# Performance work log

Hardware: AMD Instinct MI355X
Metric: run time of the kernel (lower is better)

## Reference

```python
import jax, jax.numpy as jnp
import numpy as np

NU = 30000   # n_users
NI = 15000   # n_items
D = 64       # embed_dim (== layer widths)
R = 5        # ratingClass == ratingSocial
NU5 = NU * R
NI5 = NI * R
NADJ = NU + NI5
NNZ_S = 1_200_000
NNZ_A = 840_000


def _spmm(rows, cols, vals, x, n_rows):
    # sparse (COO) matrix @ dense: out[r] = sum_e vals[e] * x[cols[e]] for rows[e]==r
    return jax.ops.segment_sum(vals[:, None] * x[cols], rows, num_segments=n_rows)


def _prelu(x, alpha):
    return jnp.where(x >= 0, x, alpha[0] * x)


def setup_inputs() -> dict:
    key = jax.random.key(0)
    ks = jax.random.split(key, 12)
    sc = lambda fan: 1.0 / np.sqrt(fan)
    return {
        "user_emb": 0.1 * jax.random.normal(ks[0], (NU5, D), jnp.float32),
        "item_emb": 0.1 * jax.random.normal(ks[1], (NI5, D), jnp.float32),
        "w_r1_w": sc(2 * D) * jax.random.normal(ks[2], (D, 2 * D), jnp.float32),
        "w_r1_b": jnp.zeros((D,), jnp.float32),
        "social_w1": sc(D) * jax.random.normal(ks[3], (D, D), jnp.float32),
        "user_w1": sc(D) * jax.random.normal(ks[4], (D, D), jnp.float32),
        "item_w1": sc(D) * jax.random.normal(ks[5], (D, D), jnp.float32),
        "alpha": jnp.full((1,), 0.25, jnp.float32),  # PReLU default init
        "social_vals": jax.random.uniform(ks[6], (NNZ_S,), jnp.float32) / 8.0,
        "adj_vals": jax.random.uniform(ks[7], (NNZ_A,), jnp.float32) / 8.0,
        "social_rows": jax.random.randint(ks[8], (NNZ_S,), 0, NU5, jnp.int32),
        "social_cols": jax.random.randint(ks[9], (NNZ_S,), 0, NU5, jnp.int32),
        "adj_rows": jax.random.randint(ks[10], (NNZ_A,), 0, NADJ, jnp.int32),
        "adj_cols": jax.random.randint(ks[11], (NNZ_A,), 0, NADJ, jnp.int32),
    }


def reference(user_emb, item_emb, w_r1_w, w_r1_b, social_w1, user_w1, item_w1,
              alpha, social_vals, adj_vals, social_rows, social_cols,
              adj_rows, adj_cols):
    # --- getSocialEmbedding ---
    e0 = _prelu(_spmm(social_rows, social_cols, social_vals, user_emb, NU5), alpha)
    e1 = _prelu(_spmm(social_rows, social_cols, social_vals, e0 @ social_w1, NU5), alpha)
    u_multi = jnp.concatenate([e0, e1], axis=1)            # (NU5, 128)
    u_social = u_multi.reshape(NU, R, 2 * D).sum(axis=1) / 4.0  # (NU, 128)

    # --- forward ---
    u = u_social @ w_r1_w.T + w_r1_b                        # Linear(128 -> 64)
    ego = jnp.concatenate([u, item_emb], axis=0)            # (NADJ, 64)
    emb = _prelu(_spmm(adj_rows, adj_cols, adj_vals, ego, NADJ), alpha)
    au0, ai0 = emb[:NU], emb[NU:]
    ego1 = jnp.concatenate([au0 @ user_w1, ai0 @ item_w1], axis=0)
    emb1 = _prelu(_spmm(adj_rows, adj_cols, adj_vals, ego1, NADJ), alpha)
    au1, ai1 = emb1[:NU], emb1[NU:]

    user_embedding = jnp.concatenate([au0, au1], axis=1)    # (NU, 128)
    item_multi = jnp.concatenate([ai0, ai1], axis=1)        # (NI5, 128)
    item_embedding = item_multi.reshape(NI, R, 2 * D).sum(axis=1) / 5.0
    return (user_embedding, item_embedding)
```

## Files before the change

### kernel.cpp

```cpp
#include <hip/hip_runtime.h>
#include <hip/hip_bf16.h>

#define NUu 30000
#define NIi 15000
#define DD 64
#define RR 5
#define NU5 150000
#define NI5 75000
#define NADJ 105000
#define NNZ_S 1200000
#define NNZ_A 840000

#define SCAN_TPB 256
#define SCAN_ELEMS 8
#define SCAN_CHUNK (SCAN_TPB * SCAN_ELEMS)

#define NBK 256
#define CHUNK 2048
#define CAP_S 10240
#define CAP_A 5120
#define NBUCK_S ((NU5 + 1023) >> 10)
#define NBUCK_A ((NADJ + 511) >> 9)

__global__ void scan_partial(const int* __restrict__ counts, int n,
                             int* __restrict__ ptr, int* __restrict__ blocksums) {
    __shared__ int sh[SCAN_TPB];
    int base = blockIdx.x * SCAN_CHUNK;
    int t = threadIdx.x;
    int loc[SCAN_ELEMS];
    int s = 0;
#pragma unroll
    for (int i = 0; i < SCAN_ELEMS; ++i) {
        int idx = base + t * SCAN_ELEMS + i;
        int v = (idx < n) ? counts[idx] : 0;
        loc[i] = s;
        s += v;
    }
    sh[t] = s;
    __syncthreads();
    for (int off = 1; off < SCAN_TPB; off <<= 1) {
        int v = (t >= off) ? sh[t - off] : 0;
        __syncthreads();
        sh[t] += v;
        __syncthreads();
    }
    int texcl = (t == 0) ? 0 : sh[t - 1];
    if (t == SCAN_TPB - 1) blocksums[blockIdx.x] = sh[t];
#pragma unroll
    for (int i = 0; i < SCAN_ELEMS; ++i) {
        int idx = base + t * SCAN_ELEMS + i;
        if (idx < n) ptr[idx] = texcl + loc[i];
    }
}

__global__ void scan_blocksums(int* __restrict__ blocksums, int nblocks) {
    __shared__ int sh[SCAN_TPB];
    int t = threadIdx.x;
    int v = (t < nblocks) ? blocksums[t] : 0;
    sh[t] = v;
    __syncthreads();
    for (int off = 1; off < SCAN_TPB; off <<= 1) {
        int u = (t >= off) ? sh[t - off] : 0;
        __syncthreads();
        sh[t] += u;
        __syncthreads();
    }
    int excl = (t == 0) ? 0 : sh[t - 1];
    if (t < nblocks) blocksums[t] = excl;
}

__global__ void scan_add(int* __restrict__ ptr, int* __restrict__ cursor, int n, int nnz,
                         const int* __restrict__ blocksums) {
    int i = blockIdx.x * blockDim.x + threadIdx.x;
    if (i < n) {
        int v = ptr[i] + blocksums[i / SCAN_CHUNK];
        ptr[i] = v;
        cursor[i] = v;
    }
    if (i == 0) ptr[n] = nnz;
}

template <int SH>
__global__ __launch_bounds__(256) void partition_edges(
    const int* __restrict__ rows, const int* __restrict__ cols,
    const float* __restrict__ vals, int nnz, int* __restrict__ counts,
    int* __restrict__ gcur, int4* __restrict__ part, int cap) {
    __shared__ int4 stage[CHUNK];
    __shared__ int hist[NBK], start[NBK], gbase[NBK], lcur[NBK];
    int t = threadIdx.x;
    int base = blockIdx.x * CHUNK;
    int nrem = nnz - base;
    int n = nrem < CHUNK ? nrem : CHUNK;
    hist[t] = 0;
    __syncthreads();
    int r[8], c[8];
    float v[8];
#pragma unroll
    for (int k = 0; k < 8; ++k) {
        int li = t + k * 256;
        if (li < n) {
            int i = base + li;
            r[k] = rows[i];
            c[k] = cols[i];
            v[k] = vals[i];
            atomicAdd(&hist[r[k] >> SH], 1);
            atomicAdd(&counts[r[k]], 1);
        } else {
            r[k] = -1;
        }
    }
    __syncthreads();
    int hv = hist[t];
    start[t] = hv;
    __syncthreads();
    for (int off = 1; off < NBK; off <<= 1) {
        int u = (t >= off) ? start[t - off] : 0;
        __syncthreads();
        start[t] += u;
        __syncthreads();
    }
    int excl = start[t] - hv;
    __syncthreads();
    start[t] = excl;
    lcur[t] = excl;
    gbase[t] = (hv > 0) ? atomicAdd(&gcur[t], hv) : 0;
    __syncthreads();
#pragma unroll
    for (int k = 0; k < 8; ++k) {
        if (r[k] >= 0) {
            int b = r[k] >> SH;
            int p = atomicAdd(&lcur[b], 1);
            stage[p] = make_int4(r[k], c[k], __float_as_int(v[k]), 0);
        }
    }
    __syncthreads();
    for (int j = t; j < n; j += 256) {
        int4 e = stage[j];
        int b = e.x >> SH;
        part[(size_t)b * cap + gbase[b] + (j - start[b])] = e;
    }
}

__global__ __launch_bounds__(256) void bucket_fill(
    const int4* __restrict__ part, const int* __restrict__ gcur, int cap,
    int* __restrict__ cursor, int2* __restrict__ ecv) {
    int b = blockIdx.x;
    int cnt = gcur[b];
    const int4* seg = part + (size_t)b * cap;
    for (int j = threadIdx.x; j < cnt; j += 256) {
        int4 e = seg[j];
        int p = atomicAdd(&cursor[e.x], 1);
        ecv[p] = make_int2(e.y, e.z);
    }
}

template <bool SPLIT>
__global__ void spmm_csr(const int* __restrict__ ptr, const int2* __restrict__ ecv,
                         const float* __restrict__ x, const float* __restrict__ x2,
                         float* __restrict__ out, int nrows) {
    int w = (blockIdx.x * blockDim.x + threadIdx.x) >> 6;
    int lane = threadIdx.x & 63;
    if (w >= nrows) return;
    int beg = ptr[w], end = ptr[w + 1];
    float a0 = 0.f, a1 = 0.f, a2 = 0.f, a3 = 0.f;
    int j = beg;
    for (; j + 3 < end; j += 4) {
        int2 e0 = ecv[j], e1 = ecv[j + 1], e2 = ecv[j + 2], e3 = ecv[j + 3];
        const float *p0, *p1, *p2, *p3;
        if (SPLIT) {
            p0 = (e0.x < NUu) ? x + (size_t)e0.x * DD : x2 + (size_t)(e0.x - NUu) * DD;
            p1 = (e1.x < NUu) ? x + (size_t)e1.x * DD : x2 + (size_t)(e1.x - NUu) * DD;
            p2 = (e2.x < NUu) ? x + (size_t)e2.x * DD : x2 + (size_t)(e2.x - NUu) * DD;
            p3 = (e3.x < NUu) ? x + (size_t)e3.x * DD : x2 + (size_t)(e3.x - NUu) * DD;
        } else {
            p0 = x + (size_t)e0.x * DD;
            p1 = x + (size_t)e1.x * DD;
            p2 = x + (size_t)e2.x * DD;
            p3 = x + (size_t)e3.x * DD;
        }
        a0 += __int_as_float(e0.y) * p0[lane];
        a1 += __int_as_float(e1.y) * p1[lane];
        a2 += __int_as_float(e2.y) * p2[lane];
        a3 += __int_as_float(e3.y) * p3[lane];
    }
    for (; j < end; ++j) {
        int2 e0 = ecv[j];
        const float* p0;
        if (SPLIT)
            p0 = (e0.x < NUu) ? x + (size_t)e0.x * DD : x2 + (size_t)(e0.x - NUu) * DD;
        else
            p0 = x + (size_t)e0.x * DD;
        a0 += __int_as_float(e0.y) * p0[lane];
    }
    out[(size_t)w * DD + lane] = (a0 + a1) + (a2 + a3);
}

__global__ void spmm_atomic(const int* __restrict__ rows, const int* __restrict__ cols,
                            const float* __restrict__ vals, const float* __restrict__ x,
                            float* __restrict__ out, int nnz) {
    int tid = blockIdx.x * blockDim.x + threadIdx.x;
    int e = tid >> 4;
    if (e >= nnz) return;
    int lc = (tid & 15) << 2;
    int r = rows[e];
    int c = cols[e];
    float v = vals[e];
    const float4 xv = *reinterpret_cast<const float4*>(x + (size_t)c * DD + lc);
    float* o = out + (size_t)r * DD + lc;
    unsafeAtomicAdd(o + 0, v * xv.x);
    unsafeAtomicAdd(o + 1, v * xv.y);
    unsafeAtomicAdd(o + 2, v * xv.z);
    unsafeAtomicAdd(o + 3, v * xv.w);
}

#define PRELU(v) ((v) >= 0.f ? (v) : alpha * (v))

__global__ void gemm64_prelu(const float* __restrict__ X, const float* __restrict__ W,
                             const float* __restrict__ alpha_p, float* __restrict__ Y,
                             int nrows) {
    __shared__ float4 Ws[64 * 16];
    int t = threadIdx.x;
    {
        const float4* Wv = (const float4*)W;
        for (int i = t; i < 1024; i += 256) Ws[i] = Wv[i];
    }
    __syncthreads();
    float alpha = alpha_p[0];
    int lane = t & 63;
    int g = t >> 6;
    int row = blockIdx.x * 64 + lane;
    if (row >= nrows) return;

    float xr[64];
    const float4* xp = (const float4*)(X + (size_t)row * DD);
#pragma unroll
    for (int i = 0; i < 16; ++i) {
        float4 v = xp[i];
        xr[4 * i + 0] = PRELU(v.x);
        xr[4 * i + 1] = PRELU(v.y);
        xr[4 * i + 2] = PRELU(v.z);
        xr[4 * i + 3] = PRELU(v.w);
    }
    float4 a0 = {0, 0, 0, 0}, a1 = a0, a2 = a0, a3 = a0;
#pragma unroll
    for (int k = 0; k < 64; ++k) {
        float xk = xr[k];
        const float4* wr = &Ws[k * 16 + g * 4];
        float4 w0 = wr[0], w1 = wr[1], w2 = wr[2], w3 = wr[3];
        a0.x += xk * w0.x; a0.y += xk * w0.y; a0.z += xk * w0.z; a0.w += xk * w0.w;
        a1.x += xk * w1.x; a1.y += xk * w1.y; a1.z += xk * w1.z; a1.w += xk * w1.w;
        a2.x += xk * w2.x; a2.y += xk * w2.y; a2.z += xk * w2.z; a2.w += xk * w2.w;
        a3.x += xk * w3.x; a3.y += xk * w3.y; a3.z += xk * w3.z; a3.w += xk * w3.w;
    }
    float4* yp = (float4*)(Y + (size_t)row * DD + g * 16);
    yp[0] = a0; yp[1] = a1; yp[2] = a2; yp[3] = a3;
}

__global__ void fuse_u(const float* __restrict__ raw0, const float* __restrict__ raw1,
                       const float* __restrict__ w_r1_w, const float* __restrict__ w_r1_b,
                       const float* __restrict__ alpha_p, float* __restrict__ uout) {
    __shared__ float Wl[128 * 68];
    int t = threadIdx.x;
    for (int i = t; i < 8192; i += 256) {
        int j = i >> 7, k = i & 127;
        Wl[k * 68 + j] = w_r1_w[i];
    }
    __syncthreads();
    float alpha = alpha_p[0];
    int lane = t & 63;
    int g = t >> 6;
    int row = blockIdx.x * 64 + lane;
    if (row >= NUu) return;

    const float4* bp = (const float4*)(w_r1_b + g * 16);
    float4 a0 = bp[0], a1 = bp[1], a2 = bp[2], a3 = bp[3];
    float xr[64];

    const float4* rp = (const float4*)(raw0 + (size_t)row * RR * DD);
#pragma unroll
    for (int i = 0; i < 16; ++i) {
        float sx = 0.f, sy = 0.f, sz = 0.f, sw = 0.f;
#pragma unroll
        for (int r = 0; r < RR; ++r) {
            float4 v = rp[r * 16 + i];
            sx += PRELU(v.x); sy += PRELU(v.y); sz += PRELU(v.z); sw += PRELU(v.w);
        }
        xr[4 * i + 0] = sx * 0.25f;
        xr[4 * i + 1] = sy * 0.25f;
        xr[4 * i + 2] = sz * 0.25f;
        xr[4 * i + 3] = sw * 0.25f;
    }
#pragma unroll
    for (int k = 0; k < 64; ++k) {
        float xk = xr[k];
        const float4* wr = (const float4*)(Wl + k * 68 + g * 16);
        float4 w0 = wr[0], w1 = wr[1], w2 = wr[2], w3 = wr[3];
        a0.x += xk * w0.x; a0.y += xk * w0.y; a0.z += xk * w0.z; a0.w += xk * w0.w;
        a1.x += xk * w1.x; a1.y += xk * w1.y; a1.z += xk * w1.z; a1.w += xk * w1.w;
        a2.x += xk * w2.x; a2.y += xk * w2.y; a2.z += xk * w2.z; a2.w += xk * w2.w;
        a3.x += xk * w3.x; a3.y += xk * w3.y; a3.z += xk * w3.z; a3.w += xk * w3.w;
    }
    rp = (const float4*)(raw1 + (size_t)row * RR * DD);
#pragma unroll
    for (int i = 0; i < 16; ++i) {
        float sx = 0.f, sy = 0.f, sz = 0.f, sw = 0.f;
#pragma unroll
        for (int r = 0; r < RR; ++r) {
            float4 v = rp[r * 16 + i];
            sx += PRELU(v.x); sy += PRELU(v.y); sz += PRELU(v.z); sw += PRELU(v.w);
        }
        xr[4 * i + 0] = sx * 0.25f;
        xr[4 * i + 1] = sy * 0.25f;
        xr[4 * i + 2] = sz * 0.25f;
        xr[4 * i + 3] = sw * 0.25f;
    }
#pragma unroll
    for (int k = 0; k < 64; ++k) {
        float xk = xr[k];
        const float4* wr = (const float4*)(Wl + (64 + k) * 68 + g * 16);
        float4 w0 = wr[0], w1 = wr[1], w2 = wr[2], w3 = wr[3];
        a0.x += xk * w0.x; a0.y += xk * w0.y; a0.z += xk * w0.z; a0.w += xk * w0.w;
        a1.x += xk * w1.x; a1.y += xk * w1.y; a1.z += xk * w1.z; a1.w += xk * w1.w;
        a2.x += xk * w2.x; a2.y += xk * w2.y; a2.z += xk * w2.z; a2.w += xk * w2.w;
        a3.x += xk * w3.x; a3.y += xk * w3.y; a3.z += xk * w3.z; a3.w += xk * w3.w;
    }
    float4* yp = (float4*)(uout + (size_t)row * DD + g * 16);
    yp[0] = a0; yp[1] = a1; yp[2] = a2; yp[3] = a3;
}

__global__ void fuse_ego1(const float* __restrict__ embraw, const float* __restrict__ Wu,
                          const float* __restrict__ Wi, const float* __restrict__ alpha_p,
                          float* __restrict__ ego1) {
    __shared__ float4 Ws[2 * 64 * 16];
    int t = threadIdx.x;
    {
        const float4* Wv = (const float4*)Wu;
        const float4* Wv2 = (const float4*)Wi;
        for (int i = t; i < 1024; i += 256) {
            Ws[i] = Wv[i];
            Ws[1024 + i] = Wv2[i];
        }
    }
    __syncthreads();
    float alpha = alpha_p[0];
    int lane = t & 63;
    int g = t >> 6;
    int row = blockIdx.x * 64 + lane;
    if (row >= NADJ) return;
    const float4* Wb = (row < NUu) ? Ws : Ws + 1024;

    float xr[64];
    const float4* xp = (const float4*)(embraw + (size_t)row * DD);
#pragma unroll
    for (int i = 0; i < 16; ++i) {
        float4 v = xp[i];
        xr[4 * i + 0] = PRELU(v.x);
        xr[4 * i + 1] = PRELU(v.y);
        xr[4 * i + 2] = PRELU(v.z);
        xr[4 * i + 3] = PRELU(v.w);
    }
    float4 a0 = {0, 0, 0, 0}, a1 = a0, a2 = a0, a3 = a0;
#pragma unroll
    for (int k = 0; k < 64; ++k) {
        float xk = xr[k];
        const float4* wr = &Wb[k * 16 + g * 4];
        float4 w0 = wr[0], w1 = wr[1], w2 = wr[2], w3 = wr[3];
        a0.x += xk * w0.x; a0.y += xk * w0.y; a0.z += xk * w0.z; a0.w += xk * w0.w;
        a1.x += xk * w1.x; a1.y += xk * w1.y; a1.z += xk * w1.z; a1.w += xk * w1.w;
        a2.x += xk * w2.x; a2.y += xk * w2.y; a2.z += xk * w2.z; a2.w += xk * w2.w;
        a3.x += xk * w3.x; a3.y += xk * w3.y; a3.z += xk * w3.z; a3.w += xk * w3.w;
    }
    float4* yp = (float4*)(ego1 + (size_t)row * DD + g * 16);
    yp[0] = a0; yp[1] = a1; yp[2] = a2; yp[3] = a3;
}

__global__ void out_combined(const float* __restrict__ embraw, const float* __restrict__ emb1raw,
                             const float* __restrict__ alpha_p, float* __restrict__ outp) {
    float alpha = alpha_p[0];
    int i = blockIdx.x * blockDim.x + threadIdx.x;
    if (i < NUu * DD) {
        int row = i >> 6, c = i & 63;
        float a = embraw[i];
        a = PRELU(a);
        float b = emb1raw[i];
        b = PRELU(b);
        outp[(size_t)row * 128 + c] = a;
        outp[(size_t)row * 128 + 64 + c] = b;
    } else {
        int i2 = i - NUu * DD;
        if (i2 >= NIi * DD) return;
        int row = i2 >> 6, c = i2 & 63;
        float s0 = 0.f, s1 = 0.f;
#pragma unroll
        for (int r = 0; r < RR; ++r) {
            size_t idx = ((size_t)NUu + (size_t)row * RR + r) * DD + c;
            float a = embraw[idx];
            s0 += PRELU(a);
            float b = emb1raw[idx];
            s1 += PRELU(b);
        }
        size_t obase = (size_t)NUu * 128 + (size_t)row * 128 + c;
        outp[obase] = s0 / 5.0f;
        outp[obase + 64] = s1 / 5.0f;
    }
}

extern "C" void kernel_launch(void* const* d_in, const int* in_sizes, int n_in,
                              void* d_out, int out_size, void* d_ws, size_t ws_size,
                              hipStream_t stream) {
    const float* user_emb  = (const float*)d_in[0];
    const float* item_emb  = (const float*)d_in[1];
    const float* w_r1_w    = (const float*)d_in[2];
    const float* w_r1_b    = (const float*)d_in[3];
    const float* social_w1 = (const float*)d_in[4];
    const float* user_w1   = (const float*)d_in[5];
    const float* item_w1   = (const float*)d_in[6];
    const float* alpha     = (const float*)d_in[7];
    const float* social_vals = (const float*)d_in[8];
    const float* adj_vals    = (const float*)d_in[9];
    const int* social_rows = (const int*)d_in[10];
    const int* social_cols = (const int*)d_in[11];
    const int* adj_rows    = (const int*)d_in[12];
    const int* adj_cols    = (const int*)d_in[13];
    float* out = (float*)d_out;

    float* A  = (float*)d_ws;
    float* B  = A + (size_t)NU5 * DD;
    float* C  = B + (size_t)NU5 * DD;
    float* Dm = C + (size_t)NU5 * DD;
    int*  s_ptr = (int*)(Dm + (size_t)NADJ * DD);
    int*  s_cur = s_ptr + (NU5 + 2);
    int2* s_ecv = (int2*)(s_cur + NU5);
    int*  a_ptr = (int*)(s_ecv + NNZ_S);
    int*  a_cur = a_ptr + (NADJ + 2);
    int2* a_ecv = (int2*)(a_cur + NADJ);
    int*  bsums = (int*)(a_ecv + NNZ_A);
    int*  gcur  = bsums + 128;
    size_t need = (size_t)((char*)(gcur + NBK) - (char*)d_ws);
    int4* part = (int4*)A;

    if (ws_size >= need) {
        hipMemsetAsync(s_cur, 0, (size_t)NU5 * sizeof(int), stream);
        hipMemsetAsync(gcur, 0, NBK * sizeof(int), stream);
        partition_edges<10><<<(NNZ_S + CHUNK - 1) / CHUNK, 256, 0, stream>>>(
            social_rows, social_cols, social_vals, NNZ_S, s_cur, gcur, part, CAP_S);
        {
            int nblocks = (NU5 + SCAN_CHUNK - 1) / SCAN_CHUNK;
            scan_partial<<<nblocks, SCAN_TPB, 0, stream>>>(s_cur, NU5, s_ptr, bsums);
            scan_blocksums<<<1, SCAN_TPB, 0, stream>>>(bsums, nblocks);
            scan_add<<<(NU5 + 255) / 256, 256, 0, stream>>>(s_ptr, s_cur, NU5, NNZ_S, bsums);
        }
        bucket_fill<<<NBUCK_S, 256, 0, stream>>>(part, gcur, CAP_S, s_cur, s_ecv);

        hipMemsetAsync(a_cur, 0, (size_t)NADJ * sizeof(int), stream);
        hipMemsetAsync(gcur, 0, NBK * sizeof(int), stream);
        partition_edges<9><<<(NNZ_A + CHUNK - 1) / CHUNK, 256, 0, stream>>>(
            adj_rows, adj_cols, adj_vals, NNZ_A, a_cur, gcur, part, CAP_A);
        {
            int nblocks = (NADJ + SCAN_CHUNK - 1) / SCAN_CHUNK;
            scan_partial<<<nblocks, SCAN_TPB, 0, stream>>>(a_cur, NADJ, a_ptr, bsums);
            scan_blocksums<<<1, SCAN_TPB, 0, stream>>>(bsums, nblocks);
            scan_add<<<(NADJ + 255) / 256, 256, 0, stream>>>(a_ptr, a_cur, NADJ, NNZ_A, bsums);
        }
        bucket_fill<<<NBUCK_A, 256, 0, stream>>>(part, gcur, CAP_A, a_cur, a_ecv);

        spmm_csr<false><<<(NU5 * 64 + 255) / 256, 256, 0, stream>>>(
            s_ptr, s_ecv, user_emb, nullptr, A, NU5);
        gemm64_prelu<<<(NU5 + 63) / 64, 256, 0, stream>>>(A, social_w1, alpha, B, NU5);
        spmm_csr<false><<<(NU5 * 64 + 255) / 256, 256, 0, stream>>>(
            s_ptr, s_ecv, B, nullptr, C, NU5);
        fuse_u<<<(NUu + 63) / 64, 256, 0, stream>>>(A, C, w_r1_w, w_r1_b, alpha, B);
        spmm_csr<true><<<(NADJ * 64 + 255) / 256, 256, 0, stream>>>(
            a_ptr, a_ecv, B, item_emb, Dm, NADJ);
        fuse_ego1<<<(NADJ + 63) / 64, 256, 0, stream>>>(Dm, user_w1, item_w1, alpha, A);
        spmm_csr<false><<<(NADJ * 64 + 255) / 256, 256, 0, stream>>>(
            a_ptr, a_ecv, A, nullptr, C, NADJ);
    } else {
        hipMemsetAsync(A, 0, (size_t)NU5 * DD * sizeof(float), stream);
        spmm_atomic<<<(NNZ_S * 16 + 255) / 256, 256, 0, stream>>>(
            social_rows, social_cols, social_vals, user_emb, A, NNZ_S);
        gemm64_prelu<<<(NU5 + 63) / 64, 256, 0, stream>>>(A, social_w1, alpha, B, NU5);
        hipMemsetAsync(C, 0, (size_t)NU5 * DD * sizeof(float), stream);
        spmm_atomic<<<(NNZ_S * 16 + 255) / 256, 256, 0, stream>>>(
            social_rows, social_cols, social_vals, B, C, NNZ_S);
        fuse_u<<<(NUu + 63) / 64, 256, 0, stream>>>(A, C, w_r1_w, w_r1_b, alpha, B);
        hipMemcpyAsync(B + (size_t)NUu * DD, item_emb, (size_t)NI5 * DD * sizeof(float),
                       hipMemcpyDeviceToDevice, stream);
        hipMemsetAsync(Dm, 0, (size_t)NADJ * DD * sizeof(float), stream);
        spmm_atomic<<<(NNZ_A * 16 + 255) / 256, 256, 0, stream>>>(
            adj_rows, adj_cols, adj_vals, B, Dm, NNZ_A);
        fuse_ego1<<<(NADJ + 63) / 64, 256, 0, stream>>>(Dm, user_w1, item_w1, alpha, A);
        hipMemsetAsync(C, 0, (size_t)NADJ * DD * sizeof(float), stream);
        spmm_atomic<<<(NNZ_A * 16 + 255) / 256, 256, 0, stream>>>(
            adj_rows, adj_cols, adj_vals, A, C, NNZ_A);
    }

    out_combined<<<((NUu + NIi) * DD + 255) / 256, 256, 0, stream>>>(Dm, C, alpha, out);
}
```

Measured before the change: 700.2 us.

## Build CSR row pointers inside bucket blocks instead of global count and scan

Drops the per-row global atomic counts and the three-kernel global prefix scan used to build CSR row pointers. Instead, a tiny scan over bucket totals gives each bucket its base offset, and each bucket block builds a shared-memory histogram of its rows, scans it, writes the row pointers, and scatters edges using shared-memory atomics. This removes global atomics, several launches and two memsets, in exchange for more shared-memory work per bucket block. scan_buckets is launched twice and its first launch reads the adjacency bucket counts before they are filled, but that output is later overwritten by the second launch.

New measurement: 595.5 us. 1.18x faster.

```diff
diff --git a/kernel.cpp b/kernel.cpp
--- a/kernel.cpp
+++ b/kernel.cpp
@@ -11,10 +11,6 @@
 #define NNZ_S 1200000
 #define NNZ_A 840000
 
-#define SCAN_TPB 256
-#define SCAN_ELEMS 8
-#define SCAN_CHUNK (SCAN_TPB * SCAN_ELEMS)
-
 #define NBK 256
 #define CHUNK 2048
 #define CAP_S 10240
@@ -22,68 +18,10 @@
 #define NBUCK_S ((NU5 + 1023) >> 10)
 #define NBUCK_A ((NADJ + 511) >> 9)
 
-__global__ void scan_partial(const int* __restrict__ counts, int n,
-                             int* __restrict__ ptr, int* __restrict__ blocksums) {
-    __shared__ int sh[SCAN_TPB];
-    int base = blockIdx.x * SCAN_CHUNK;
-    int t = threadIdx.x;
-    int loc[SCAN_ELEMS];
-    int s = 0;
-#pragma unroll
-    for (int i = 0; i < SCAN_ELEMS; ++i) {
-        int idx = base + t * SCAN_ELEMS + i;
-        int v = (idx < n) ? counts[idx] : 0;
-        loc[i] = s;
-        s += v;
-    }
-    sh[t] = s;
-    __syncthreads();
-    for (int off = 1; off < SCAN_TPB; off <<= 1) {
-        int v = (t >= off) ? sh[t - off] : 0;
-        __syncthreads();
-        sh[t] += v;
-        __syncthreads();
-    }
-    int texcl = (t == 0) ? 0 : sh[t - 1];
-    if (t == SCAN_TPB - 1) blocksums[blockIdx.x] = sh[t];
-#pragma unroll
-    for (int i = 0; i < SCAN_ELEMS; ++i) {
-        int idx = base + t * SCAN_ELEMS + i;
-        if (idx < n) ptr[idx] = texcl + loc[i];
-    }
-}
-
-__global__ void scan_blocksums(int* __restrict__ blocksums, int nblocks) {
-    __shared__ int sh[SCAN_TPB];
-    int t = threadIdx.x;
-    int v = (t < nblocks) ? blocksums[t] : 0;
-    sh[t] = v;
-    __syncthreads();
-    for (int off = 1; off < SCAN_TPB; off <<= 1) {
-        int u = (t >= off) ? sh[t - off] : 0;
-        __syncthreads();
-        sh[t] += u;
-        __syncthreads();
-    }
-    int excl = (t == 0) ? 0 : sh[t - 1];
-    if (t < nblocks) blocksums[t] = excl;
-}
-
-__global__ void scan_add(int* __restrict__ ptr, int* __restrict__ cursor, int n, int nnz,
-                         const int* __restrict__ blocksums) {
-    int i = blockIdx.x * blockDim.x + threadIdx.x;
-    if (i < n) {
-        int v = ptr[i] + blocksums[i / SCAN_CHUNK];
-        ptr[i] = v;
-        cursor[i] = v;
-    }
-    if (i == 0) ptr[n] = nnz;
-}
-
 template <int SH>
 __global__ __launch_bounds__(256) void partition_edges(
     const int* __restrict__ rows, const int* __restrict__ cols,
-    const float* __restrict__ vals, int nnz, int* __restrict__ counts,
+    const float* __restrict__ vals, int nnz,
     int* __restrict__ gcur, int4* __restrict__ part, int cap) {
     __shared__ int4 stage[CHUNK];
     __shared__ int hist[NBK], start[NBK], gbase[NBK], lcur[NBK];
@@ -104,7 +42,6 @@
             c[k] = cols[i];
             v[k] = vals[i];
             atomicAdd(&hist[r[k] >> SH], 1);
-            atomicAdd(&counts[r[k]], 1);
         } else {
             r[k] = -1;
         }
@@ -141,15 +78,78 @@
     }
 }
 
-__global__ __launch_bounds__(256) void bucket_fill(
-    const int4* __restrict__ part, const int* __restrict__ gcur, int cap,
-    int* __restrict__ cursor, int2* __restrict__ ecv) {
+__global__ void scan_buckets(const int* __restrict__ gcur_s, int* __restrict__ gbase_s,
+                             int* __restrict__ sptr,
+                             const int* __restrict__ gcur_a, int* __restrict__ gbase_a,
+                             int* __restrict__ aptr) {
+    __shared__ int sh[256];
+    int t = threadIdx.x;
+    const int* gc = (blockIdx.x == 0) ? gcur_s : gcur_a;
+    int* gb = (blockIdx.x == 0) ? gbase_s : gbase_a;
+    int nb = (blockIdx.x == 0) ? NBUCK_S : NBUCK_A;
+    int v = (t < nb) ? gc[t] : 0;
+    sh[t] = v;
+    __syncthreads();
+    for (int off = 1; off < 256; off <<= 1) {
+        int u = (t >= off) ? sh[t - off] : 0;
+        __syncthreads();
+        sh[t] += u;
+        __syncthreads();
+    }
+    if (t < nb) gb[t] = sh[t] - v;
+    if (t == 0) {
+        if (blockIdx.x == 0) sptr[NU5] = NNZ_S;
+        else aptr[NADJ] = NNZ_A;
+    }
+}
+
+template <int SH>
+__global__ __launch_bounds__(256) void bucket_sort_fill(
+    const int4* __restrict__ part, const int* __restrict__ gcur,
+    const int* __restrict__ gbase, int cap, int nrows,
+    int* __restrict__ ptr, int2* __restrict__ ecv) {
+    constexpr int NR = 1 << SH;
+    constexpr int E = NR / 256;
+    __shared__ int hist[NR];
+    __shared__ int tsum[256];
     int b = blockIdx.x;
+    int t = threadIdx.x;
+    int base_r = b << SH;
     int cnt = gcur[b];
+    int gb = gbase[b];
     const int4* seg = part + (size_t)b * cap;
-    for (int j = threadIdx.x; j < cnt; j += 256) {
+#pragma unroll
+    for (int i = 0; i < E; ++i) hist[t * E + i] = 0;
+    __syncthreads();
+    for (int j = t; j < cnt; j += 256) atomicAdd(&hist[seg[j].x - base_r], 1);
+    __syncthreads();
+    int loc[E];
+    int s = 0;
+#pragma unroll
+    for (int i = 0; i < E; ++i) {
+        loc[i] = s;
+        s += hist[t * E + i];
+    }
+    tsum[t] = s;
+    __syncthreads();
+    for (int off = 1; off < 256; off <<= 1) {
+        int u = (t >= off) ? tsum[t - off] : 0;
+        __syncthreads();
+        tsum[t] += u;
+        __syncthreads();
+    }
+    int texcl = (t == 0) ? 0 : tsum[t - 1];
+#pragma unroll
+    for (int i = 0; i < E; ++i) {
+        int excl = texcl + loc[i];
+        int row = base_r + t * E + i;
+        if (row < nrows) ptr[row] = gb + excl;
+        hist[t * E + i] = excl;
+    }
+    __syncthreads();
+    for (int j = t; j < cnt; j += 256) {
         int4 e = seg[j];
-        int p = atomicAdd(&cursor[e.x], 1);
+        int p = gb + atomicAdd(&hist[e.x - base_r], 1);
         ecv[p] = make_int2(e.y, e.z);
     }
 }
@@ -429,40 +429,30 @@
     float* C  = B + (size_t)NU5 * DD;
     float* Dm = C + (size_t)NU5 * DD;
     int*  s_ptr = (int*)(Dm + (size_t)NADJ * DD);
-    int*  s_cur = s_ptr + (NU5 + 2);
-    int2* s_ecv = (int2*)(s_cur + NU5);
+    int2* s_ecv = (int2*)(s_ptr + (NU5 + 2));
     int*  a_ptr = (int*)(s_ecv + NNZ_S);
-    int*  a_cur = a_ptr + (NADJ + 2);
-    int2* a_ecv = (int2*)(a_cur + NADJ);
-    int*  bsums = (int*)(a_ecv + NNZ_A);
-    int*  gcur  = bsums + 128;
-    size_t need = (size_t)((char*)(gcur + NBK) - (char*)d_ws);
+    int2* a_ecv = (int2*)(a_ptr + (NADJ + 2));
+    int*  gcur_s  = (int*)(a_ecv + NNZ_A);
+    int*  gcur_a  = gcur_s + NBK;
+    int*  gbase_s = gcur_a + NBK;
+    int*  gbase_a = gbase_s + NBK;
+    size_t need = (size_t)((char*)(gbase_a + NBK) - (char*)d_ws);
     int4* part = (int4*)A;
 
     if (ws_size >= need) {
-        hipMemsetAsync(s_cur, 0, (size_t)NU5 * sizeof(int), stream);
-        hipMemsetAsync(gcur, 0, NBK * sizeof(int), stream);
+        hipMemsetAsync(gcur_s, 0, 2 * NBK * sizeof(int), stream);
         partition_edges<10><<<(NNZ_S + CHUNK - 1) / CHUNK, 256, 0, stream>>>(
-            social_rows, social_cols, social_vals, NNZ_S, s_cur, gcur, part, CAP_S);
-        {
-            int nblocks = (NU5 + SCAN_CHUNK - 1) / SCAN_CHUNK;
-            scan_partial<<<nblocks, SCAN_TPB, 0, stream>>>(s_cur, NU5, s_ptr, bsums);
-            scan_blocksums<<<1, SCAN_TPB, 0, stream>>>(bsums, nblocks);
-            scan_add<<<(NU5 + 255) / 256, 256, 0, stream>>>(s_ptr, s_cur, NU5, NNZ_S, bsums);
-        }
-        bucket_fill<<<NBUCK_S, 256, 0, stream>>>(part, gcur, CAP_S, s_cur, s_ecv);
-
-        hipMemsetAsync(a_cur, 0, (size_t)NADJ * sizeof(int), stream);
-        hipMemsetAsync(gcur, 0, NBK * sizeof(int), stream);
+            social_rows, social_cols, social_vals, NNZ_S, gcur_s, part, CAP_S);
+        scan_buckets<<<2, 256, 0, stream>>>(gcur_s, gbase_s, s_ptr,
+                                            gcur_a, gbase_a, a_ptr);
+        bucket_sort_fill<10><<<NBUCK_S, 256, 0, stream>>>(
+            part, gcur_s, gbase_s, CAP_S, NU5, s_ptr, s_ecv);
         partition_edges<9><<<(NNZ_A + CHUNK - 1) / CHUNK, 256, 0, stream>>>(
-            adj_rows, adj_cols, adj_vals, NNZ_A, a_cur, gcur, part, CAP_A);
-        {
-            int nblocks = (NADJ + SCAN_CHUNK - 1) / SCAN_CHUNK;
-            scan_partial<<<nblocks, SCAN_TPB, 0, stream>>>(a_cur, NADJ, a_ptr, bsums);
-            scan_blocksums<<<1, SCAN_TPB, 0, stream>>>(bsums, nblocks);
-            scan_add<<<(NADJ + 255) / 256, 256, 0, stream>>>(a_ptr, a_cur, NADJ, NNZ_A, bsums);
-        }
-        bucket_fill<<<NBUCK_A, 256, 0, stream>>>(part, gcur, CAP_A, a_cur, a_ecv);
+            adj_rows, adj_cols, adj_vals, NNZ_A, gcur_a, part, CAP_A);
+        scan_buckets<<<2, 256, 0, stream>>>(gcur_s, gbase_s, s_ptr,
+                                            gcur_a, gbase_a, a_ptr);
+        bucket_sort_fill<9><<<NBUCK_A, 256, 0, stream>>>(
+            part, gcur_a, gbase_a, CAP_A, NADJ, a_ptr, a_ecv);
 
         spmm_csr<false><<<(NU5 * 64 + 255) / 256, 256, 0, stream>>>(
             s_ptr, s_ecv, user_emb, nullptr, A, NU5);
```
